# Performance work log

Hardware: AMD Instinct MI355X
Metric: run time of the kernel (lower is better)

## Reference

```python
import jax, jax.numpy as jnp
import numpy as np

N, E, F_IN, G = 50000, 800000, 128, 256
LAYERS = [(128, 4, 64), (256, 4, 64), (256, 1, 64)]  # (fan_in, heads, per-head dim)


def setup_inputs() -> dict:
    key = jax.random.key(0)
    ks = iter(jax.random.split(key, 64))
    nrm = lambda shp, s=1.0: jax.random.normal(next(ks), shp, jnp.float32) * s
    d = {}
    d["x"] = nrm((N, F_IN))
    d["edge_index"] = jax.random.randint(next(ks), (2, E), 0, N, dtype=jnp.int32)
    d["batch"] = jnp.sort(jax.random.randint(next(ks), (N,), 0, G, dtype=jnp.int32))
    for i, (fin, h, c) in enumerate(LAYERS):
        d[f"w{i}"] = nrm((fin, h * c), 1.0 / np.sqrt(fin))
        d[f"asrc{i}"] = nrm((h, c), 0.1)
        d[f"adst{i}"] = nrm((h, c), 0.1)
        d[f"b{i}"] = nrm((h * c,), 0.1)
        d[f"g{i}"] = 1.0 + nrm((h * c,), 0.1)
        d[f"be{i}"] = nrm((h * c,), 0.1)
        d[f"m{i}"] = nrm((h * c,), 0.1)
        d[f"v{i}"] = jnp.abs(nrm((h * c,), 0.1)) + 1.0
    d["fc1w"] = nrm((192, 64), 1.0 / np.sqrt(192)); d["fc1b"] = nrm((64,), 0.1)
    d["fc2w"] = nrm((64, 32), 1.0 / np.sqrt(64));   d["fc2b"] = nrm((32,), 0.1)
    d["fc3w"] = nrm((32, 1), 1.0 / np.sqrt(32));    d["fc3b"] = nrm((1,), 0.1)
    return d


def _gat_layer(x, w, a_s, a_d, b, src, dst, n, heads):
    c = w.shape[1] // heads
    h = (x @ w).reshape(n, heads, c)                      # [N,H,C]
    al_s = jnp.sum(h * a_s[None], axis=-1)                # [N,H]
    al_d = jnp.sum(h * a_d[None], axis=-1)                # [N,H]
    e = jax.nn.leaky_relu(al_s[src] + al_d[dst], 0.2)     # [E',H]
    emax = jax.ops.segment_max(e, dst, num_segments=n)
    emax = jnp.where(jnp.isfinite(emax), emax, 0.0)
    ee = jnp.exp(e - emax[dst])
    den = jax.ops.segment_sum(ee, dst, num_segments=n)
    alpha = ee / (den[dst] + 1e-16)                       # edge softmax per dst node
    out = jax.ops.segment_sum(h[src] * alpha[..., None], dst, num_segments=n)
    return out.reshape(n, heads * c) + b


def _bn(x, g, be, m, v):
    return (x - m) * jax.lax.rsqrt(v + 1e-5) * g + be


def reference(x, edge_index, batch,
              w0, asrc0, adst0, b0, g0, be0, m0, v0,
              w1, asrc1, adst1, b1, g1, be1, m1, v1,
              w2, asrc2, adst2, b2, g2, be2, m2, v2,
              fc1w, fc1b, fc2w, fc2b, fc3w, fc3b):
    n = x.shape[0]
    loop = jnp.arange(n, dtype=edge_index.dtype)          # add_self_loops (PyG default)
    src = jnp.concatenate([edge_index[0], loop])
    dst = jnp.concatenate([edge_index[1], loop])
    layers = [(w0, asrc0, adst0, b0, g0, be0, m0, v0, 4),
              (w1, asrc1, adst1, b1, g1, be1, m1, v1, 4),
              (w2, asrc2, adst2, b2, g2, be2, m2, v2, 1)]
    for (w, a_s, a_d, b, g, be, m, v, heads) in layers:
        x = _gat_layer(x, w, a_s, a_d, b, src, dst, n, heads)
        x = jax.nn.elu(_bn(x, g, be, m, v))
    # multi-pool readout over graphs
    xsum = jax.ops.segment_sum(x, batch, num_segments=G)
    cnt = jax.ops.segment_sum(jnp.ones((n, 1), x.dtype), batch, num_segments=G)
    xmean = xsum / jnp.maximum(cnt, 1.0)
    xmax = jax.ops.segment_max(x, batch, num_segments=G)
    xmax = jnp.where(jnp.isfinite(xmax), xmax, 0.0)
    h = jnp.concatenate([xmean, xmax, xsum], axis=1)      # [G, 192]
    h = jax.nn.relu(h @ fc1w + fc1b)
    h = jax.nn.relu(h @ fc2w + fc2b)
    return h @ fc3w + fc3b                                # [G, 1]
```

## Files before the change

kernel.cpp:

```cpp
#include <hip/hip_runtime.h>
#include <hip/hip_fp16.h>

typedef unsigned short ushort_t;
typedef unsigned int uint_t;
typedef __attribute__((ext_vector_type(8))) _Float16 half8;
typedef __attribute__((ext_vector_type(4))) float f32x4;

#define NN 50000
#define NE 800000
#define NGR 256

typedef __attribute__((address_space(3))) unsigned int as3_u32;
typedef const __attribute__((address_space(1))) unsigned int as1_u32c;
__device__ __forceinline__ void gld16(const ushort_t* g, void* lds_base) {
    __builtin_amdgcn_global_load_lds((as1_u32c*)g, (as3_u32*)lds_base, 16, 0, 0);
}

__global__ void k_scan1(const int* __restrict__ deg, int* __restrict__ rowp,
                        int* __restrict__ bsum, int M) {
    __shared__ int sm[256];
    int t = threadIdx.x, i = blockIdx.x * 256 + t;
    int v = (i < M) ? deg[i] + 1 : 0;
    sm[t] = v; __syncthreads();
    for (int off = 1; off < 256; off <<= 1) {
        int x = (t >= off) ? sm[t - off] : 0;
        __syncthreads();
        sm[t] += x;
        __syncthreads();
    }
    if (i < M) rowp[i] = sm[t] - v;
    if (t == 255) bsum[blockIdx.x] = sm[255];
}

__global__ void k_scan2(int* bsum, int NB) {
    __shared__ int sm[256];
    int t = threadIdx.x;
    int v = (t < NB) ? bsum[t] : 0;
    sm[t] = v; __syncthreads();
    for (int off = 1; off < 256; off <<= 1) {
        int x = (t >= off) ? sm[t - off] : 0;
        __syncthreads();
        sm[t] += x;
        __syncthreads();
    }
    if (t < NB) bsum[t] = sm[t] - v;
}

__global__ void k_scan3(int* rowp, const int* __restrict__ bsum, int* __restrict__ cur,
                        int M, int total) {
    int i = blockIdx.x * 256 + threadIdx.x;
    if (i < M) { rowp[i] += bsum[blockIdx.x]; cur[i] = 0; }
    if (i == 0) rowp[M] = total;
}

__global__ void k_fill(const int* __restrict__ src, const int* __restrict__ dst,
                       const int* __restrict__ rowp, int* __restrict__ cur,
                       int* __restrict__ colv, int E, int M) {
    int i = blockIdx.x * 256 + threadIdx.x;
    if (i < E) {
        int d = dst[i];
        int pos = rowp[d] + atomicAdd(&cur[d], 1);
        colv[pos] = src[i];
    } else if (i < E + M) {
        int nn = i - E;
        int pos = rowp[nn] + atomicAdd(&cur[nn], 1);
        colv[pos] = nn;
    }
}

__global__ void k_prep(const float* __restrict__ x0, __half* __restrict__ xf,
                       const float* __restrict__ W0, const float* __restrict__ W1,
                       const float* __restrict__ W2, __half* __restrict__ th,
                       const int* __restrict__ edst, int* __restrict__ deg) {
    int i = blockIdx.x * 256 + threadIdx.x;
    if (i < 1600000) {
        float4 v = ((const float4*)x0)[i];
        __half2 a = __floats2half2_rn(v.x, v.y);
        __half2 b = __floats2half2_rn(v.z, v.w);
        *(__half2*)(xf + i * 4) = a;
        *(__half2*)(xf + i * 4 + 2) = b;
    } else if (i < 1600000 + 114688) {
        int w = i - 1600000;
        const float* W; int K, NC, idx, base;
        if (w < 32768)      { W = W0; K = 128; NC = 256; idx = w;         base = 0; }
        else if (w < 98304) { W = W1; K = 256; NC = 256; idx = w - 32768; base = 32768; }
        else                { W = W2; K = 256; NC = 64;  idx = w - 98304; base = 98304; }
        int k = idx / NC, n = idx % NC;
        th[base + n * K + k] = __float2half(W[idx]);
    } else if (i < 1600000 + 114688 + NE) {
        atomicAdd(&deg[edst[i - 1714688]], 1);
    }
}

template<int KD, int BN>
__global__ __launch_bounds__(256)
void k_mgemm(const __half* __restrict__ Ax, const __half* __restrict__ Bth,
             __half* __restrict__ Hout,
             const float* __restrict__ a_s, const float* __restrict__ a_d,
             float* __restrict__ als, float* __restrict__ ald,
             int H, int M, int NC) {
    constexpr int BM = 128, BK = 32;
    __shared__ ushort_t sA[BM * BK];
    __shared__ ushort_t sB[BN * BK];
    const int tid = threadIdx.x;
    const int m0 = blockIdx.x * BM;
    const int n0 = blockIdx.y * BN;
    const int wv = tid >> 6, ln = tid & 63;
    const int lrow = ln & 15, lq = ln >> 4;
    constexpr int RT = (BN == 128) ? 4 : 2;
    int wm, wn;
    if constexpr (BN == 128) { wm = (wv >> 1) * 64; wn = (wv & 1) * 64; }
    else                     { wm = wv * 32;        wn = 0; }
    const int roff = ln >> 2;
    const int coff = (ln & 3) * 8;

    f32x4 acc[RT][4] = {};

    for (int k0 = 0; k0 < KD; k0 += BK) {
        #pragma unroll
        for (int ch = 0; ch < 2; ++ch) {
            int rb = wv * 32 + ch * 16;
            size_t ga = (size_t)(m0 + rb + roff) * KD + k0 + coff;
            gld16((const ushort_t*)Ax + ga, &sA[rb * BK]);
        }
        if constexpr (BN == 128) {
            #pragma unroll
            for (int ch = 0; ch < 2; ++ch) {
                int rb = wv * 32 + ch * 16;
                size_t gb = (size_t)(n0 + rb + roff) * KD + k0 + coff;
                gld16((const ushort_t*)Bth + gb, &sB[rb * BK]);
            }
        } else {
            int rb = wv * 16;
            size_t gb = (size_t)(n0 + rb + roff) * KD + k0 + coff;
            gld16((const ushort_t*)Bth + gb, &sB[rb * BK]);
        }
        __syncthreads();
        half8 af[RT], bf[4];
        #pragma unroll
        for (int r = 0; r < RT; ++r)
            af[r] = *(const half8*)&sA[(wm + r * 16 + lrow) * BK + lq * 8];
        #pragma unroll
        for (int c = 0; c < 4; ++c)
            bf[c] = *(const half8*)&sB[(wn + c * 16 + lrow) * BK + lq * 8];
        #pragma unroll
        for (int r = 0; r < RT; ++r)
            #pragma unroll
            for (int c = 0; c < 4; ++c)
                acc[r][c] = __builtin_amdgcn_mfma_f32_16x16x32_f16(af[r], bf[c], acc[r][c], 0, 0, 0);
        __syncthreads();
    }
    #pragma unroll
    for (int r = 0; r < RT; ++r) {
        #pragma unroll
        for (int c = 0; c < 4; ++c) {
            int colg = n0 + wn + c * 16 + lrow;
            #pragma unroll
            for (int j = 0; j < 4; ++j) {
                int row = m0 + wm + r * 16 + lq * 4 + j;
                if (row < M) Hout[(size_t)row * NC + colg] = __float2half(acc[r][c][j]);
            }
        }
    }
    int hh = (n0 + wn) >> 6;
    float asv[4], adv[4];
    #pragma unroll
    for (int c = 0; c < 4; ++c) {
        int cg = (n0 + wn + c * 16 + lrow) & 63;
        asv[c] = a_s[hh * 64 + cg];
        adv[c] = a_d[hh * 64 + cg];
    }
    #pragma unroll
    for (int r = 0; r < RT; ++r) {
        #pragma unroll
        for (int j = 0; j < 4; ++j) {
            float ts = 0.f, td = 0.f;
            #pragma unroll
            for (int c = 0; c < 4; ++c) {
                float v = acc[r][c][j];
                ts += v * asv[c];
                td += v * adv[c];
            }
            #pragma unroll
            for (int m = 1; m < 16; m <<= 1) {
                ts += __shfl_xor(ts, m);
                td += __shfl_xor(td, m);
            }
            int row = m0 + wm + r * 16 + lq * 4 + j;
            if (lrow == 0 && row < M) {
                als[row * H + hh] = ts;
                ald[row * H + hh] = td;
            }
        }
    }
}

template<int H>
__global__ __launch_bounds__(256)
void k_att(const float* __restrict__ als, const float* __restrict__ ald,
           const int* __restrict__ rowp, const int* __restrict__ colv,
           __half* __restrict__ alpha, float* __restrict__ invb, int M) {
    int node = blockIdx.x * 16 + (threadIdx.x >> 4);
    if (node >= M) return;
    int l = threadIdx.x & 15;
    int rs = rowp[node], re = rowp[node + 1];
    if constexpr (H == 4) {
        float4 ad = *(const float4*)(ald + node * 4);
        float d0 = 0.f, d1 = 0.f, d2 = 0.f, d3 = 0.f;
        for (int i = rs + l; i < re; i += 16) {
            int s = colv[i];
            float4 av = *(const float4*)(als + s * 4);
            float e0 = av.x + ad.x; e0 = e0 > 0.f ? e0 : 0.2f * e0; e0 = __expf(e0);
            float e1 = av.y + ad.y; e1 = e1 > 0.f ? e1 : 0.2f * e1; e1 = __expf(e1);
            float e2 = av.z + ad.z; e2 = e2 > 0.f ? e2 : 0.2f * e2; e2 = __expf(e2);
            float e3 = av.w + ad.w; e3 = e3 > 0.f ? e3 : 0.2f * e3; e3 = __expf(e3);
            d0 += e0; d1 += e1; d2 += e2; d3 += e3;
            __half2 p0 = __floats2half2_rn(e0, e1);
            __half2 p1 = __floats2half2_rn(e2, e3);
            uint2 pk;
            pk.x = *(uint_t*)&p0; pk.y = *(uint_t*)&p1;
            *(uint2*)(alpha + (size_t)i * 4) = pk;
        }
        #pragma unroll
        for (int off = 1; off < 16; off <<= 1) {
            d0 += __shfl_xor(d0, off); d1 += __shfl_xor(d1, off);
            d2 += __shfl_xor(d2, off); d3 += __shfl_xor(d3, off);
        }
        if (l == 0)
            *(float4*)(invb + node * 4) = make_float4(1.f / (d0 + 1e-16f), 1.f / (d1 + 1e-16f),
                                                      1.f / (d2 + 1e-16f), 1.f / (d3 + 1e-16f));
    } else {
        float ad = ald[node];
        float d = 0.f;
        for (int i = rs + l; i < re; i += 16) {
            int s = colv[i];
            float e = als[s] + ad; e = e > 0.f ? e : 0.2f * e; e = __expf(e);
            d += e;
            alpha[i] = __float2half(e);
        }
        #pragma unroll
        for (int off = 1; off < 16; off <<= 1) d += __shfl_xor(d, off);
        if (l == 0) invb[node] = 1.f / (d + 1e-16f);
    }
}

template<int H, bool SPLIT>
__global__ __launch_bounds__(256)
void k_agg(const __half* __restrict__ h, const __half* __restrict__ alpha,
           const float* __restrict__ invb, const int* __restrict__ rowp,
           const int* __restrict__ colv,
           const float* __restrict__ bias, const float* __restrict__ gam,
           const float* __restrict__ bet, const float* __restrict__ mu,
           const float* __restrict__ var,
           __half* __restrict__ xo, float* __restrict__ xf, int M) {
    constexpr int HC = H * 64;
    constexpr int EG = 512 / HC;
    constexpr int L  = 64 / EG;
    constexpr int UN = (H == 4) ? 4 : 2;
    int node = blockIdx.x * 4 + (threadIdx.x >> 6);
    if (node >= M) return;
    int lane = threadIdx.x & 63;
    int rs = rowp[node], re = rowp[node + 1];
    int l = lane & (L - 1), eg = lane / L;
    int hB = (l * 8) >> 6;
    const ushort_t* ab = (const ushort_t*)alpha;
    float acc[8] = {};
    for (int i = rs; i < re; i += EG * UN) {
        #pragma unroll
        for (int k = 0; k < UN; ++k) {
            int idx = i + eg + k * EG;
            bool vld = idx < re;
            int idx2 = vld ? idx : rs;
            int s = colv[idx2];
            ushort_t abits;
            if constexpr (H == 4) abits = ab[(size_t)idx2 * 4 + hB];
            else                  abits = ab[idx2];
            float a = __half2float(__ushort_as_half(vld ? abits : (ushort_t)0));
            uint4 hv = *(const uint4*)(h + (size_t)s * HC + l * 8);
            const __half* hp = (const __half*)&hv;
            #pragma unroll
            for (int j = 0; j < 8; ++j)
                acc[j] = fmaf(a, __half2float(hp[j]), acc[j]);
        }
    }
    #pragma unroll
    for (int off = L; off < 64; off <<= 1) {
        #pragma unroll
        for (int j = 0; j < 8; ++j) acc[j] += __shfl_xor(acc[j], off);
    }
    if (eg == 0) {
        float inv = (H == 4) ? invb[node * 4 + hB] : invb[node];
        float fo[8];
        #pragma unroll
        for (int j = 0; j < 8; ++j) {
            int d = l * 8 + j;
            float o = acc[j] * inv + bias[d];
            float bn = (o - mu[d]) * rsqrtf(var[d] + 1e-5f) * gam[d] + bet[d];
            fo[j] = bn > 0.f ? bn : (__expf(bn) - 1.f);
        }
        if constexpr (SPLIT) {
            __half2 p0 = __floats2half2_rn(fo[0], fo[1]);
            __half2 p1 = __floats2half2_rn(fo[2], fo[3]);
            __half2 p2 = __floats2half2_rn(fo[4], fo[5]);
            __half2 p3 = __floats2half2_rn(fo[6], fo[7]);
            uint4 pk;
            pk.x = *(uint_t*)&p0; pk.y = *(uint_t*)&p1;
            pk.z = *(uint_t*)&p2; pk.w = *(uint_t*)&p3;
            *(uint4*)&xo[(size_t)node * HC + l * 8] = pk;
        } else {
            *(float4*)&xf[(size_t)node * HC + l * 8] = make_float4(fo[0], fo[1], fo[2], fo[3]);
            *(float4*)&xf[(size_t)node * HC + l * 8 + 4] = make_float4(fo[4], fo[5], fo[6], fo[7]);
        }
    }
}

__global__ __launch_bounds__(512)
void k_poolfc(const float* __restrict__ x, const int* __restrict__ batch,
              const float* __restrict__ fc1w, const float* __restrict__ fc1b,
              const float* __restrict__ fc2w, const float* __restrict__ fc2b,
              const float* __restrict__ fc3w, const float* __restrict__ fc3b,
              float* __restrict__ out, int M) {
    __shared__ float ssum[8][64];
    __shared__ float smax[8][64];
    __shared__ float hb[192];
    __shared__ float h1[64];
    __shared__ float h2[32];
    int g = blockIdx.x, t = threadIdx.x;
    int d = t & 63, sub = t >> 6;
    int lo = 0, hi = M;
    while (lo < hi) { int mid = (lo + hi) >> 1; if (batch[mid] < g) lo = mid + 1; else hi = mid; }
    int s = lo;
    lo = 0; hi = M;
    while (lo < hi) { int mid = (lo + hi) >> 1; if (batch[mid] < g + 1) lo = mid + 1; else hi = mid; }
    int e = lo;
    float sum = 0.f, mx = -3.0e38f;
    for (int n = s + sub; n < e; n += 8) {
        float v = x[(size_t)n * 64 + d];
        sum += v; mx = fmaxf(mx, v);
    }
    ssum[sub][d] = sum; smax[sub][d] = mx;
    __syncthreads();
    if (t < 64) {
        float sm = 0.f, m2 = -3.0e38f;
        #pragma unroll
        for (int k = 0; k < 8; ++k) { sm += ssum[k][t]; m2 = fmaxf(m2, smax[k][t]); }
        int cnt = e - s;
        hb[t] = sm / (float)(cnt > 1 ? cnt : 1);
        hb[64 + t] = (cnt == 0) ? 0.f : m2;
        hb[128 + t] = sm;
    }
    __syncthreads();
    if (t < 64) {
        float s1 = fc1b[t];
        for (int k = 0; k < 192; ++k) s1 += hb[k] * fc1w[k * 64 + t];
        h1[t] = fmaxf(s1, 0.f);
    }
    __syncthreads();
    if (t < 32) {
        float s2 = fc2b[t];
        for (int k = 0; k < 64; ++k) s2 += h1[k] * fc2w[k * 32 + t];
        h2[t] = fmaxf(s2, 0.f);
    }
    __syncthreads();
    if (t == 0) {
        float s3 = fc3b[0];
        for (int k = 0; k < 32; ++k) s3 += h2[k] * fc3w[k];
        out[g] = s3;
    }
}

extern "C" void kernel_launch(void* const* d_in, const int* in_sizes, int n_in,
                              void* d_out, int out_size, void* d_ws, size_t ws_size,
                              hipStream_t stream) {
    const float* x0     = (const float*)d_in[0];
    const int* ei       = (const int*)d_in[1];
    const int* batch    = (const int*)d_in[2];
    const float* W[3]   = {(const float*)d_in[3],  (const float*)d_in[11], (const float*)d_in[19]};
    const float* AS[3]  = {(const float*)d_in[4],  (const float*)d_in[12], (const float*)d_in[20]};
    const float* AD[3]  = {(const float*)d_in[5],  (const float*)d_in[13], (const float*)d_in[21]};
    const float* BI[3]  = {(const float*)d_in[6],  (const float*)d_in[14], (const float*)d_in[22]};
    const float* GA[3]  = {(const float*)d_in[7],  (const float*)d_in[15], (const float*)d_in[23]};
    const float* BE[3]  = {(const float*)d_in[8],  (const float*)d_in[16], (const float*)d_in[24]};
    const float* MU[3]  = {(const float*)d_in[9],  (const float*)d_in[17], (const float*)d_in[25]};
    const float* VA[3]  = {(const float*)d_in[10], (const float*)d_in[18], (const float*)d_in[26]};
    const float* fc1w = (const float*)d_in[27];
    const float* fc1b = (const float*)d_in[28];
    const float* fc2w = (const float*)d_in[29];
    const float* fc2b = (const float*)d_in[30];
    const float* fc3w = (const float*)d_in[31];
    const float* fc3b = (const float*)d_in[32];

    char* ws = (char*)d_ws;
    int*   rowp   = (int*)  (ws);
    int*   colv   = (int*)  (ws + 200704);
    int*   bsum   = (int*)  (ws + 3600704);
    float* als    = (float*)(ws + 3602432);
    int*   cur    = (int*)  (ws + 3602432);
    float* ald    = (float*)(ws + 4402432);
    __half* wTh   = (__half*)(ws + 5202432);
    __half* h_buf = (__half*)(ws + 5661184);
    __half* xf16  = (__half*)(ws + 31261184);
    float* xpool  = (float*)(ws + 56885760);
    __half* alpha = (__half*)(ws + 69685760);
    float* invb   = (float*)(ws + 83285760);

    const int* esrc = ei;
    const int* edst = ei + NE;
    const int NB_SCAN = (NN + 255) / 256;

    hipMemsetAsync(cur, 0, NN * sizeof(int), stream);
    k_prep<<<(1600000 + 114688 + NE + 255) / 256, 256, 0, stream>>>(x0, xf16, W[0], W[1], W[2],
                                                                    wTh, edst, cur);
    k_scan1<<<NB_SCAN, 256, 0, stream>>>(cur, rowp, bsum, NN);
    k_scan2<<<1, 256, 0, stream>>>(bsum, NB_SCAN);
    k_scan3<<<NB_SCAN, 256, 0, stream>>>(rowp, bsum, cur, NN, NE + NN);
    k_fill<<<(NE + NN + 255) / 256, 256, 0, stream>>>(esrc, edst, rowp, cur, colv, NE, NN);

    const int GB = (NN + 127) / 128;
    int nwb = (NN + 3) / 4;
    int nab = (NN + 15) / 16;

    k_mgemm<128, 128><<<dim3(GB, 2), 256, 0, stream>>>(xf16, wTh, h_buf,
                                                       AS[0], AD[0], als, ald, 4, NN, 256);
    k_att<4><<<nab, 256, 0, stream>>>(als, ald, rowp, colv, alpha, invb, NN);
    k_agg<4, true><<<nwb, 256, 0, stream>>>(h_buf, alpha, invb, rowp, colv,
                                            BI[0], GA[0], BE[0], MU[0], VA[0],
                                            xf16, nullptr, NN);
    k_mgemm<256, 128><<<dim3(GB, 2), 256, 0, stream>>>(xf16, wTh + 32768, h_buf,
                                                       AS[1], AD[1], als, ald, 4, NN, 256);
    k_att<4><<<nab, 256, 0, stream>>>(als, ald, rowp, colv, alpha, invb, NN);
    k_agg<4, true><<<nwb, 256, 0, stream>>>(h_buf, alpha, invb, rowp, colv,
                                            BI[1], GA[1], BE[1], MU[1], VA[1],
                                            xf16, nullptr, NN);
    k_mgemm<256, 64><<<dim3(GB, 1), 256, 0, stream>>>(xf16, wTh + 98304, h_buf,
                                                      AS[2], AD[2], als, ald, 1, NN, 64);
    k_att<1><<<nab, 256, 0, stream>>>(als, ald, rowp, colv, alpha, invb, NN);
    k_agg<1, false><<<nwb, 256, 0, stream>>>(h_buf, alpha, invb, rowp, colv,
                                             BI[2], GA[2], BE[2], MU[2], VA[2],
                                             nullptr, xpool, NN);

    k_poolfc<<<NGR, 512, 0, stream>>>(xpool, batch, fc1w, fc1b, fc2w, fc2b, fc3w, fc3b,
                                      (float*)d_out, NN);
    (void)in_sizes; (void)n_in; (void)out_size; (void)ws_size;
}
```

Measured before the change: 475.0 us.

## Fuse CSR fill into first-layer GEMM launch to overlap independent work

Result: faster. 453.4 us (-4.5%).

```diff
diff --git a/kernel.cpp b/kernel.cpp
--- a/kernel.cpp
+++ b/kernel.cpp
@@ -51,21 +51,6 @@
     int i = blockIdx.x * 256 + threadIdx.x;
     if (i < M) { rowp[i] += bsum[blockIdx.x]; cur[i] = 0; }
     if (i == 0) rowp[M] = total;
-}
-
-__global__ void k_fill(const int* __restrict__ src, const int* __restrict__ dst,
-                       const int* __restrict__ rowp, int* __restrict__ cur,
-                       int* __restrict__ colv, int E, int M) {
-    int i = blockIdx.x * 256 + threadIdx.x;
-    if (i < E) {
-        int d = dst[i];
-        int pos = rowp[d] + atomicAdd(&cur[d], 1);
-        colv[pos] = src[i];
-    } else if (i < E + M) {
-        int nn = i - E;
-        int pos = rowp[nn] + atomicAdd(&cur[nn], 1);
-        colv[pos] = nn;
-    }
 }
 
 __global__ void k_prep(const float* __restrict__ x0, __half* __restrict__ xf,
@@ -93,18 +78,17 @@
 }
 
 template<int KD, int BN>
-__global__ __launch_bounds__(256)
-void k_mgemm(const __half* __restrict__ Ax, const __half* __restrict__ Bth,
-             __half* __restrict__ Hout,
-             const float* __restrict__ a_s, const float* __restrict__ a_d,
-             float* __restrict__ als, float* __restrict__ ald,
-             int H, int M, int NC) {
+__device__ __forceinline__ void gemm_body(int bx, int by,
+    const __half* __restrict__ Ax, const __half* __restrict__ Bth,
+    __half* __restrict__ Hout, const float* __restrict__ a_s,
+    const float* __restrict__ a_d, float* __restrict__ als,
+    float* __restrict__ ald, int H, int M, int NC) {
     constexpr int BM = 128, BK = 32;
     __shared__ ushort_t sA[BM * BK];
     __shared__ ushort_t sB[BN * BK];
     const int tid = threadIdx.x;
-    const int m0 = blockIdx.x * BM;
-    const int n0 = blockIdx.y * BN;
+    const int m0 = bx * BM;
+    const int n0 = by * BN;
     const int wv = tid >> 6, ln = tid & 63;
     const int lrow = ln & 15, lq = ln >> 4;
     constexpr int RT = (BN == 128) ? 4 : 2;
@@ -191,6 +175,41 @@
                 als[row * H + hh] = ts;
                 ald[row * H + hh] = td;
             }
+        }
+    }
+}
+
+template<int KD, int BN>
+__global__ __launch_bounds__(256)
+void k_mgemm(const __half* __restrict__ Ax, const __half* __restrict__ Bth,
+             __half* __restrict__ Hout,
+             const float* __restrict__ a_s, const float* __restrict__ a_d,
+             float* __restrict__ als, float* __restrict__ ald,
+             int H, int M, int NC) {
+    gemm_body<KD, BN>(blockIdx.x, blockIdx.y, Ax, Bth, Hout, a_s, a_d, als, ald, H, M, NC);
+}
+
+__global__ __launch_bounds__(256)
+void k_gf(const __half* __restrict__ Ax, const __half* __restrict__ Bth,
+          __half* __restrict__ Hout,
+          const float* __restrict__ a_s, const float* __restrict__ a_d,
+          float* __restrict__ als, float* __restrict__ ald, int M,
+          const int* __restrict__ esrc, const int* __restrict__ edst,
+          const int* __restrict__ rowp, int* __restrict__ cur,
+          int* __restrict__ colv) {
+    if (blockIdx.x < 782) {
+        gemm_body<128, 128>(blockIdx.x >> 1, blockIdx.x & 1, Ax, Bth, Hout,
+                            a_s, a_d, als, ald, 4, M, 256);
+    } else {
+        int i = (blockIdx.x - 782) * 256 + threadIdx.x;
+        if (i < NE) {
+            int d = edst[i];
+            int pos = rowp[d] + atomicAdd(&cur[d], 1);
+            colv[pos] = esrc[i];
+        } else if (i < NE + NN) {
+            int nn = i - NE;
+            int pos = rowp[nn] + atomicAdd(&cur[nn], 1);
+            colv[pos] = nn;
         }
     }
 }
@@ -395,7 +414,6 @@
     int*   colv   = (int*)  (ws + 200704);
     int*   bsum   = (int*)  (ws + 3600704);
     float* als    = (float*)(ws + 3602432);
-    int*   cur    = (int*)  (ws + 3602432);
     float* ald    = (float*)(ws + 4402432);
     __half* wTh   = (__half*)(ws + 5202432);
     __half* h_buf = (__half*)(ws + 5661184);
@@ -403,6 +421,7 @@
     float* xpool  = (float*)(ws + 56885760);
     __half* alpha = (__half*)(ws + 69685760);
     float* invb   = (float*)(ws + 83285760);
+    int*   cur    = (int*)  (ws + 84085760);
 
     const int* esrc = ei;
     const int* edst = ei + NE;
@@ -414,14 +433,14 @@
     k_scan1<<<NB_SCAN, 256, 0, stream>>>(cur, rowp, bsum, NN);
     k_scan2<<<1, 256, 0, stream>>>(bsum, NB_SCAN);
     k_scan3<<<NB_SCAN, 256, 0, stream>>>(rowp, bsum, cur, NN, NE + NN);
-    k_fill<<<(NE + NN + 255) / 256, 256, 0, stream>>>(esrc, edst, rowp, cur, colv, NE, NN);
 
     const int GB = (NN + 127) / 128;
+    const int FILLB = (NE + NN + 255) / 256;
     int nwb = (NN + 3) / 4;
     int nab = (NN + 15) / 16;
 
-    k_mgemm<128, 128><<<dim3(GB, 2), 256, 0, stream>>>(xf16, wTh, h_buf,
-                                                       AS[0], AD[0], als, ald, 4, NN, 256);
+    k_gf<<<782 + FILLB, 256, 0, stream>>>(xf16, wTh, h_buf, AS[0], AD[0], als, ald, NN,
+                                          esrc, edst, rowp, cur, colv);
     k_att<4><<<nab, 256, 0, stream>>>(als, ald, rowp, colv, alpha, invb, NN);
     k_agg<4, true><<<nwb, 256, 0, stream>>>(h_buf, alpha, invb, rowp, colv,
                                             BI[0], GA[0], BE[0], MU[0], VA[0],
```
